# Performance work log

Hardware: AMD Instinct MI355X
Metric: run time of the kernel (lower is better)

Reference implementation:

```python
import jax, jax.numpy as jnp
import numpy as np
from jax import lax

B, C, N, COUT, H, W = 8, 64, 16, 3, 96, 96
EPS = 1e-5  # torch GroupNorm / InstanceNorm2d default eps


def group_norm(x, gamma, beta, groups):
    n, c, h, w = x.shape
    xg = x.reshape(n, groups, c // groups, h, w)
    mu = xg.mean((2, 3, 4), keepdims=True)
    var = xg.var((2, 3, 4), keepdims=True)
    xg = (xg - mu) / jnp.sqrt(var + EPS)
    return xg.reshape(n, c, h, w) * gamma[None, :, None, None] + beta[None, :, None, None]


def instance_norm(x, gamma, beta):
    mu = x.mean((2, 3), keepdims=True)
    var = x.var((2, 3), keepdims=True)
    return (x - mu) / jnp.sqrt(var + EPS) * gamma[None, :, None, None] + beta[None, :, None, None]


def conv3x3(x, w, b):
    y = lax.conv_general_dilated(x, w, (1, 1), 'SAME',
                                 dimension_numbers=('NCHW', 'OIHW', 'NCHW'))
    return y + b[None, :, None, None]


def setup_inputs() -> dict:
    key = jax.random.key(0)
    ks = jax.random.split(key, 8)
    p = {}
    p['sr'] = jax.random.normal(ks[0], (B, C, H, W), jnp.float32)
    p['tg'] = jax.random.normal(ks[1], (B, C, H, W), jnp.float32)
    # self.w : Conv2d(c, c*n, 1) -> 1x1 conv == matmul over channels
    p['w_w'] = jax.random.normal(ks[2], (C * N, C), jnp.float32) * 0.05
    p['w_b'] = jnp.zeros((C * N,), jnp.float32)
    # mask_block: GN(c//4,c), ReLU, Conv(c,64,3), GN(16,64), ReLU, Conv(64,1,3)
    p['gn1_g'] = jnp.ones((C,), jnp.float32)
    p['gn1_b'] = jnp.zeros((C,), jnp.float32)
    p['c1_w'] = jax.random.normal(ks[3], (64, C, 3, 3), jnp.float32) * 0.05
    p['c1_b'] = jnp.zeros((64,), jnp.float32)
    p['gn2_g'] = jnp.ones((64,), jnp.float32)
    p['gn2_b'] = jnp.zeros((64,), jnp.float32)
    p['c2_w'] = jax.random.normal(ks[4], (1, 64, 3, 3), jnp.float32) * 0.05
    p['c2_b'] = jnp.zeros((1,), jnp.float32)
    # gen_block: IN(n), ReLU, Conv(n,n,1), IN(n), ReLU, Conv(n,cout,1)
    p['in1_g'] = jnp.ones((N,), jnp.float32)
    p['in1_b'] = jnp.zeros((N,), jnp.float32)
    p['c3_w'] = jax.random.normal(ks[5], (N, N), jnp.float32) * 0.1
    p['c3_b'] = jnp.zeros((N,), jnp.float32)
    p['in2_g'] = jnp.ones((N,), jnp.float32)
    p['in2_b'] = jnp.zeros((N,), jnp.float32)
    p['c4_w'] = jax.random.normal(ks[6], (COUT, N), jnp.float32) * 0.1
    p['c4_b'] = jnp.zeros((COUT,), jnp.float32)
    return p


def reference(sr, tg, w_w, w_b, gn1_g, gn1_b, c1_w, c1_b, gn2_g, gn2_b,
              c2_w, c2_b, in1_g, in1_b, c3_w, c3_b, in2_g, in2_b, c4_w, c4_b):
    b, c, h, w = sr.shape
    n = N
    # 1x1 conv then view to capsule layout [b, n, c, h*w]
    s = jnp.einsum('oc,bchw->bohw', w_w, sr) + w_b[None, :, None, None]
    s = s.reshape(b, n, c, h * w)
    op = s.sum(3, keepdims=True)  # [b,n,c,1]
    cof = None
    for _ in range(3):  # fixed 3-step dynamic routing
        opn = op / jnp.maximum(jnp.linalg.norm(op, axis=2, keepdims=True), 1e-12)
        cof = jax.nn.softmax((s * opn).sum(2, keepdims=True), axis=3)  # [b,n,1,hw]
        op = (s * cof).sum(3, keepdims=True)  # [b,n,c,1]
    # broadcast capsule vectors onto target feature map
    msk_tg = (tg[:, None, :, :, :] + op[:, :, :, :, None]).reshape(b * n, c, h, w)
    x = group_norm(msk_tg, gn1_g, gn1_b, c // 4)
    x = conv3x3(jax.nn.relu(x), c1_w, c1_b)
    x = group_norm(x, gn2_g, gn2_b, 64 // 4)
    x = conv3x3(jax.nn.relu(x), c2_w, c2_b)  # [b*n,1,h,w]
    msk = x.reshape(b, n, h, w)
    # spatial center-of-mass loss
    hw_cof = jax.nn.softmax(msk.reshape(b, n, h * w), -1).reshape(b, n, h, w)[..., None]
    hw_idx = jnp.stack(jnp.meshgrid(jnp.linspace(-1.0, 1.0, h),
                                    jnp.linspace(-1.0, 1.0, w), indexing='ij'), -1)[None, None]
    hw_centr = (hw_cof * hw_idx).sum((2, 3), keepdims=True)  # [b,n,1,1,2]
    centr_loss = (hw_cof * (hw_idx - hw_centr) ** 2).sum((2, 3, 4)).mean()
    # gen_block + sigmoid activation
    g = instance_norm(msk, in1_g, in1_b)
    g = jnp.einsum('on,bnhw->bohw', c3_w, jax.nn.relu(g)) + c3_b[None, :, None, None]
    g = instance_norm(g, in2_g, in2_b)
    rec = jax.nn.sigmoid(jnp.einsum('on,bnhw->bohw', c4_w, jax.nn.relu(g)) + c4_b[None, :, None, None])
    # outer product capsule x mask: [b,n,c,1] x [b,n,h,w] -> [b,n,c,h,w]
    op_out = jnp.einsum('bnc,bnhw->bnchw', op[..., 0], msk)
    return (op_out, msk, rec, centr_loss, cof.reshape(b, n, h, w))
```

## Files before the change

kernel.cpp:

```cpp
#include <hip/hip_runtime.h>
#include <math.h>

#define BB 8
#define CC 64
#define NCAP 16
#define HH 96
#define WW 96
#define PP (HH*WW)
#define BNN (BB*NCAP)
#define EPSN 1e-5f

typedef short short8 __attribute__((ext_vector_type(8)));
typedef unsigned short u16x8 __attribute__((ext_vector_type(8)));
typedef unsigned short u16x4 __attribute__((ext_vector_type(4)));
typedef float float4v __attribute__((ext_vector_type(4)));

__device__ __forceinline__ float bf2f(unsigned short u){
  union{unsigned int i; float f;} x; x.i = ((unsigned int)u)<<16; return x.f;
}
__device__ __forceinline__ unsigned short f2bf(float f){
  union{float f; unsigned int i;} x; x.f=f;
  unsigned int r = x.i + 0x7fffu + ((x.i>>16)&1u);
  return (unsigned short)(r>>16);
}
__device__ __forceinline__ float4v mfma16(short8 a, short8 b, float4v c){
  return __builtin_amdgcn_mfma_f32_16x16x32_bf16(a, b, c, 0, 0, 0);
}

__device__ __forceinline__ float blkred_sum(float v, float* red4){
  int tid = threadIdx.x; int lane = tid & 63, wv = tid >> 6;
  #pragma unroll
  for (int off=32; off>0; off>>=1) v += __shfl_down(v, off, 64);
  __syncthreads();
  if (lane == 0) red4[wv] = v;
  __syncthreads();
  return red4[0] + red4[1] + red4[2] + red4[3];
}
__device__ __forceinline__ float blkred_max(float v, float* red4){
  int tid = threadIdx.x; int lane = tid & 63, wv = tid >> 6;
  #pragma unroll
  for (int off=32; off>0; off>>=1) v = fmaxf(v, __shfl_down(v, off, 64));
  __syncthreads();
  if (lane == 0) red4[wv] = v;
  __syncthreads();
  return fmaxf(fmaxf(red4[0], red4[1]), fmaxf(red4[2], red4[3]));
}

__global__ void kpre_tgt(const float* __restrict__ tg, unsigned short* __restrict__ tgt){
  int b = blockIdx.x/36, pc = blockIdx.x - (blockIdx.x/36)*36;
  int p = pc*256 + threadIdx.x;
  unsigned short vals[CC];
  #pragma unroll 8
  for (int c=0;c<CC;c++) vals[c] = f2bf(tg[((size_t)b*CC + c)*PP + p]);
  u16x8* dst = (u16x8*)&tgt[((size_t)b*PP + p)*CC];
  #pragma unroll
  for (int j=0;j<8;j++){
    u16x8 v;
    #pragma unroll
    for (int e=0;e<8;e++) v[e] = vals[j*8+e];
    dst[j] = v;
  }
}

__global__ void kw_bf16(const float* __restrict__ w1, unsigned short* __restrict__ Wt){
  int i = blockIdx.x*256 + threadIdx.x;
  int o = i/576; int rem = i - o*576; int c = rem/9; int tap = rem - c*9;
  Wt[(tap*CC + o)*CC + c] = f2bf(w1[i]);
}

__global__ void k0_colstats(const float* __restrict__ sr, const float* __restrict__ tg,
                            float* __restrict__ t, float* __restrict__ S1, float* __restrict__ S2){
  int row = blockIdx.x;
  const float* srp = sr + (size_t)row * PP;
  const float* tgp = tg + (size_t)row * PP;
  float s0=0.f, a1=0.f, a2=0.f;
  for (int p = threadIdx.x; p < PP; p += 256){
    s0 += srp[p];
    float v = tgp[p];
    a1 += v; a2 += v*v;
  }
  __shared__ float red4[4];
  s0 = blkred_sum(s0, red4);
  a1 = blkred_sum(a1, red4);
  a2 = blkred_sum(a2, red4);
  if (threadIdx.x == 0){ t[row]=s0; S1[row]=a1; S2[row]=a2; }
}

__global__ void k_update(const float* __restrict__ Wm, const float* __restrict__ wb,
                         const float* __restrict__ vec, float biasmul, int perB,
                         float* __restrict__ opv, float* __restrict__ uv, float* __restrict__ bu){
  int bn = blockIdx.x; int n = bn & (NCAP-1); int b = bn >> 4;
  int c = threadIdx.x;
  __shared__ float Wsh[CC*65];
  __shared__ float vsh[CC];
  __shared__ float opsh[CC];
  vsh[c] = perB ? vec[b*CC + c] : vec[bn*CC + c];
  const float* Wn = Wm + (size_t)n*CC*CC;
  for (int i=c;i<CC*CC;i+=64){ int r=i>>6, k=i&63; Wsh[r*65+k]=Wn[i]; }
  __syncthreads();
  float acc = biasmul * wb[n*CC + c];
  #pragma unroll 8
  for (int k=0;k<CC;k++) acc += Wsh[c*65+k]*vsh[k];
  opv[bn*CC+c] = acc;
  float ss = acc*acc;
  #pragma unroll
  for (int off=32;off>0;off>>=1) ss += __shfl_down(ss, off, 64);
  ss = __shfl(ss, 0, 64);
  float inv = 1.0f / fmaxf(sqrtf(ss), 1e-12f);
  opsh[c] = acc * inv;
  __syncthreads();
  float uacc = 0.f;
  #pragma unroll 8
  for (int k=0;k<CC;k++) uacc += opsh[k] * Wsh[k*65+c];
  uv[bn*CC+c] = uacc;
  float bb = opsh[c]*wb[n*CC+c];
  #pragma unroll
  for (int off=32;off>0;off>>=1) bb += __shfl_down(bb, off, 64);
  if (c==0) bu[bn] = bb;
}

__global__ __launch_bounds__(128) void k2f_dpass(
    const float* __restrict__ sr, const float* __restrict__ uv,
    const float* __restrict__ bu, float* __restrict__ dbuf,
    float* __restrict__ partm, float* __restrict__ partz,
    float* __restrict__ prt, int writed){
  int b = blockIdx.x / 72; int pc = blockIdx.x - b*72;
  int tid = threadIdx.x;
  int p = pc*128 + tid;
  __shared__ float ush[NCAP][CC];
  __shared__ float bush[NCAP];
  __shared__ float msh[NCAP];
  __shared__ float wsh[NCAP*132];
  __shared__ float srsh[CC*132];
  for (int i=tid;i<NCAP*CC;i+=128) ush[i>>6][i&63] = uv[b*NCAP*CC + i];
  if (tid < NCAP) bush[tid] = bu[b*NCAP+tid];
  __syncthreads();
  float acc[NCAP];
  #pragma unroll
  for (int n=0;n<NCAP;n++) acc[n]=bush[n];
  #pragma unroll 4
  for (int c=0;c<CC;c++){
    float v = sr[((size_t)b*CC + c)*PP + p];
    srsh[c*132+tid] = v;
    #pragma unroll
    for (int n=0;n<NCAP;n++) acc[n] += ush[n][c]*v;
  }
  #pragma unroll
  for (int n=0;n<NCAP;n++){
    wsh[n*132+tid] = acc[n];
    if (writed) dbuf[((size_t)(b*NCAP+n))*PP + p] = acc[n];
  }
  __syncthreads();
  {
    int n = tid >> 3, seg = tid & 7;
    float m = -1e30f;
    #pragma unroll
    for (int i=0;i<16;i++) m = fmaxf(m, wsh[n*132+seg*16+i]);
    #pragma unroll
    for (int off=1; off<8; off<<=1) m = fmaxf(m, __shfl_xor(m, off, 64));
    float z = 0.f;
    #pragma unroll
    for (int i=0;i<16;i++) z += __expf(wsh[n*132+seg*16+i] - m);
    #pragma unroll
    for (int off=1; off<8; off<<=1) z += __shfl_xor(z, off, 64);
    if (seg == 0){
      partm[(b*NCAP + n)*72 + pc] = m;
      partz[(b*NCAP + n)*72 + pc] = z;
      msh[n] = m;
    }
  }
  __syncthreads();
  #pragma unroll
  for (int n=0;n<NCAP;n++) wsh[n*132+tid] = __expf(wsh[n*132+tid]-msh[n]);
  __syncthreads();
  {
    int c = tid & 63, half = tid >> 6;
    float acc8[8];
    #pragma unroll
    for (int i=0;i<8;i++) acc8[i]=0.f;
    const float4* sp = (const float4*)&srsh[c*132];
    #pragma unroll 4
    for (int k=0;k<32;k++){
      float4 sv = sp[k];
      #pragma unroll
      for (int i=0;i<8;i++){
        float4 wv = *(const float4*)&wsh[(half*8+i)*132+4*k];
        acc8[i] += wv.x*sv.x + wv.y*sv.y + wv.z*sv.z + wv.w*sv.w;
      }
    }
    float* pb = prt + (((size_t)b*72+pc)*NCAP + half*8)*CC + c;
    #pragma unroll
    for (int i=0;i<8;i++) pb[(size_t)i*CC] = acc8[i];
  }
}

__global__ void k_iter(const float* __restrict__ prt, const float* __restrict__ partm,
                       const float* __restrict__ partz, const float* __restrict__ Wm,
                       const float* __restrict__ wb, float* __restrict__ mrow,
                       float* __restrict__ zrow, float* __restrict__ opv,
                       float* __restrict__ uv, float* __restrict__ bu){
  int bn = blockIdx.x; int n = bn & (NCAP-1); int b = bn >> 4;
  int c = threadIdx.x;
  float m1 = partm[bn*72 + c];
  float m2 = (c < 8) ? partm[bn*72 + 64 + c] : -1e30f;
  float mm = fmaxf(m1, m2);
  #pragma unroll
  for (int off=32;off>0;off>>=1) mm = fmaxf(mm, __shfl_xor(mm, off, 64));
  float z = partz[bn*72 + c]*__expf(m1 - mm);
  if (c < 8) z += partz[bn*72 + 64 + c]*__expf(m2 - mm);
  #pragma unroll
  for (int off=32;off>0;off>>=1) z += __shfl_xor(z, off, 64);
  if (c==0){ mrow[bn]=mm; zrow[bn]=z; }
  float invZ = 1.0f/z;
  float s = 0.f;
  #pragma unroll 8
  for (int pc=0;pc<72;pc++){
    float w = __expf(partm[bn*72+pc] - mm);
    s += prt[(((size_t)b*72+pc)*NCAP + n)*CC + c] * w;
  }
  float rvc = s*invZ;
  __shared__ float Wsh[CC*65];
  __shared__ float vsh[CC];
  __shared__ float opsh[CC];
  vsh[c] = rvc;
  const float* Wn = Wm + (size_t)n*CC*CC;
  for (int i=c;i<CC*CC;i+=64){ int r=i>>6, k=i&63; Wsh[r*65+k]=Wn[i]; }
  __syncthreads();
  float acc = wb[n*CC + c];
  #pragma unroll 8
  for (int k=0;k<CC;k++) acc += Wsh[c*65+k]*vsh[k];
  opv[bn*CC+c] = acc;
  float ss = acc*acc;
  #pragma unroll
  for (int off=32;off>0;off>>=1) ss += __shfl_down(ss, off, 64);
  ss = __shfl(ss, 0, 64);
  float inv = 1.0f / fmaxf(sqrtf(ss), 1e-12f);
  opsh[c] = acc * inv;
  __syncthreads();
  float uacc = 0.f;
  #pragma unroll 8
  for (int k=0;k<CC;k++) uacc += opsh[k] * Wsh[k*65+c];
  uv[bn*CC+c] = uacc;
  float bb = opsh[c]*wb[n*CC+c];
  #pragma unroll
  for (int off=32;off>0;off>>=1) bb += __shfl_down(bb, off, 64);
  if (c==0) bu[bn] = bb;
}

__global__ void k6_cofout(const float* __restrict__ dbuf, const float* __restrict__ mrow,
                          const float* __restrict__ zrow, float* __restrict__ cof){
  int bn = blockIdx.y;
  int p = blockIdx.x*256 + threadIdx.x;
  float m=mrow[bn], invz=1.0f/zrow[bn];
  cof[(size_t)bn*PP+p] = __expf(dbuf[(size_t)bn*PP+p]-m)*invz;
}

__global__ void k7_gn1(const float* __restrict__ S1, const float* __restrict__ S2,
                       const float* __restrict__ opv, const float* __restrict__ g1,
                       const float* __restrict__ b1, float* __restrict__ Aaff,
                       float* __restrict__ Daff, float* __restrict__ gn2s,
                       float* __restrict__ gn2q, float* __restrict__ in2s,
                       float* __restrict__ in2q, float* __restrict__ lossout){
  int bn = blockIdx.x; int b = bn >> 4;
  int c = threadIdx.x;
  __shared__ float e1[CC], e2[CC], mu[16], ri[16];
  float op = opv[bn*CC+c];
  float s1 = S1[b*CC+c], s2 = S2[b*CC+c];
  e1[c] = s1 + (float)PP*op;
  e2[c] = s2 + 2.0f*op*s1 + (float)PP*op*op;
  __syncthreads();
  if (c < 16){
    float m  = (e1[4*c]+e1[4*c+1]+e1[4*c+2]+e1[4*c+3])*(1.0f/(4.0f*PP));
    float qq = (e2[4*c]+e2[4*c+1]+e2[4*c+2]+e2[4*c+3])*(1.0f/(4.0f*PP));
    mu[c]=m; ri[c]=rsqrtf(qq-m*m+EPSN);
    gn2s[bn*16+c]=0.f; gn2q[bn*16+c]=0.f;
  }
  if (bn==0){
    in2s[c]=0.f; in2s[CC+c]=0.f; in2q[c]=0.f; in2q[CC+c]=0.f;
    if (c==0) lossout[0]=0.f;
  }
  __syncthreads();
  int g = c>>2;
  float A = ri[g]*g1[c];
  Aaff[bn*CC+c]=A;
  Daff[bn*CC+c]=(op-mu[g])*A + b1[c];
}

__global__ __launch_bounds__(256, 6) void k8_conv1_mfma(
    const unsigned short* __restrict__ tgt, const unsigned short* __restrict__ Wt,
    const float* __restrict__ c1b, const float* __restrict__ Aaff,
    const float* __restrict__ Daff, unsigned short* __restrict__ y1b,
    float* __restrict__ gn2s, float* __restrict__ gn2q){
  int blk = blockIdx.x;
  int bn = blk/72, tt = blk - bn*72;
  int ty = tt/6, tx = tt - ty*6;
  int y0 = ty*8, x0 = tx*16;
  int b = bn >> 4;
  int tid = threadIdx.x, w = tid>>6, lane = tid&63, quad = lane>>4, col16 = lane&15;

  __shared__ unsigned short xh[10*18*72];
  __shared__ float Ash[CC], Dsh[CC];
  if (tid < CC){ Ash[tid]=Aaff[bn*CC+tid]; Dsh[tid]=Daff[bn*CC+tid]; }
  __syncthreads();

  const unsigned short* tgb = tgt + (size_t)b*PP*CC;
  for (int task = tid; task < 1440; task += 256){
    int j = task & 7, pi = task >> 3;
    int row = pi/18, col = pi - row*18;
    int gy = y0 + row - 1, gx = x0 + col - 1;
    u16x8 ov;
    if ((unsigned)gy < (unsigned)HH && (unsigned)gx < (unsigned)WW){
      u16x8 iv = *(const u16x8*)(tgb + ((size_t)(gy*WW+gx))*CC + j*8);
      #pragma unroll
      for (int e=0;e<8;e++){
        float f = bf2f(iv[e]);
        f = fmaxf(Ash[j*8+e]*f + Dsh[j*8+e], 0.f);
        ov[e] = f2bf(f);
      }
    } else {
      #pragma unroll
      for (int e=0;e<8;e++) ov[e]=0;
    }
    *(u16x8*)&xh[(row*18+col)*72 + j*8] = ov;
  }
  __syncthreads();

  float4v acc[4][2];
  #pragma unroll
  for (int mt=0;mt<4;mt++)
    #pragma unroll
    for (int ri=0;ri<2;ri++)
      #pragma unroll
      for (int e=0;e<4;e++) acc[mt][ri][e]=0.f;

  const unsigned short* xb0 = &xh[((2*w)*18 + col16)*72 + quad*8];
  const unsigned short* wbase = Wt + (size_t)(col16*CC + quad*8);
  #pragma unroll
  for (int tap=0; tap<9; ++tap){
    const int dy = tap/3, dx = tap - (tap/3)*3;
    const int toff = (dy*18 + dx)*72;
    #pragma unroll
    for (int chunk=0; chunk<2; ++chunk){
      short8 a[4];
      #pragma unroll
      for (int mt=0;mt<4;mt++)
        a[mt] = *(const short8*)(wbase + tap*4096 + mt*1024 + chunk*32);
      short8 bf[2];
      #pragma unroll
      for (int ri=0;ri<2;ri++)
        bf[ri] = *(const short8*)(xb0 + toff + ri*(18*72) + chunk*32);
      #pragma unroll
      for (int mt=0;mt<4;mt++)
        #pragma unroll
        for (int ri=0;ri<2;ri++)
          acc[mt][ri] = mfma16(a[mt], bf[ri], acc[mt][ri]);
    }
  }

  __syncthreads();
  unsigned short* ybuf = xh;
  #pragma unroll
  for (int mt=0;mt<4;mt++){
    float gs=0.f, gq=0.f;
    #pragma unroll
    for (int ri=0;ri<2;ri++){
      u16x4 pv;
      #pragma unroll
      for (int e=0;e<4;e++){
        int o = mt*16 + quad*4 + e;
        float v = acc[mt][ri][e] + c1b[o];
        pv[e] = f2bf(v);
        gs += v; gq += v*v;
      }
      *(u16x4*)&ybuf[((2*w+ri)*16 + col16)*72 + mt*16 + quad*4] = pv;
    }
    #pragma unroll
    for (int off=1; off<16; off<<=1){
      gs += __shfl_xor(gs, off, 64);
      gq += __shfl_xor(gq, off, 64);
    }
    if (col16==0){
      atomicAdd(&gn2s[bn*16 + mt*4 + quad], gs);
      atomicAdd(&gn2q[bn*16 + mt*4 + quad], gq);
    }
  }
  __syncthreads();
  unsigned short* ybn = y1b + (size_t)bn*PP*CC;
  #pragma unroll
  for (int pass=0; pass<4; ++pass){
    int row = pass*2 + (tid>>7);
    int chunk = tid & 127;
    int pix = row*16 + (chunk>>3), c8 = chunk&7;
    u16x8 v = *(const u16x8*)&ybuf[pix*72 + c8*8];
    *(u16x8*)&ybn[(size_t)((y0+row)*WW + x0)*CC + chunk*8] = v;
  }
}

__global__ __launch_bounds__(256) void k10_conv2(
    const unsigned short* __restrict__ y1b, const float* __restrict__ w2,
    const float* __restrict__ b2, const float* __restrict__ gn2s,
    const float* __restrict__ gn2q, const float* __restrict__ g2c,
    const float* __restrict__ b2c, float* __restrict__ mskout){
  int blk=blockIdx.x; int bn=blk/36; int tt=blk-bn*36;
  int y0=(tt/3)*8, x0=(tt%3)*32;
  int tid=threadIdx.x;
  __shared__ unsigned short xh2[10*34*72];
  __shared__ float wsh2[CC*9];
  __shared__ float Ash[CC], Dsh[CC];
  __shared__ float mg[16], rg[16];
  for (int i=tid;i<CC*9;i+=256) wsh2[i]=w2[i];
  if (tid<16){
    float m = gn2s[bn*16+tid]*(1.0f/(4.0f*PP));
    float q = gn2q[bn*16+tid]*(1.0f/(4.0f*PP));
    mg[tid]=m; rg[tid]=rsqrtf(q-m*m+EPSN);
  }
  __syncthreads();
  if (tid<CC){
    float A = rg[tid>>2]*g2c[tid];
    Ash[tid]=A; Dsh[tid]=b2c[tid]-mg[tid>>2]*A;
  }

  const unsigned short* yb = y1b + (size_t)bn*PP*CC;
  for (int task=tid; task<2720; task+=256){
    int j = task & 7, pi = task >> 3;
    int row = pi/34, col = pi - row*34;
    int gy = y0 + row - 1, gx = x0 + col - 1;
    u16x8 iv;
    if ((unsigned)gy < (unsigned)HH && (unsigned)gx < (unsigned)WW){
      iv = *(const u16x8*)(yb + ((size_t)(gy*WW+gx))*CC + j*8);
    } else {
      #pragma unroll
      for (int e=0;e<8;e++) iv[e]=0;
    }
    *(u16x8*)&xh2[(row*34+col)*72 + j*8] = iv;
  }
  __syncthreads();

  int xi = tid&31, yi = tid>>5;
  float acc = 0.f;
  for (int t=0; t<9; ++t){
    int kh = t/3, kw = t - kh*3;
    int gy2 = y0 + yi + kh - 1, gx2 = x0 + xi + kw - 1;
    if ((unsigned)gy2 < (unsigned)HH && (unsigned)gx2 < (unsigned)WW){
      const unsigned short* px = &xh2[((yi+kh)*34 + xi+kw)*72];
      #pragma unroll
      for (int oct=0; oct<8; ++oct){
        u16x8 v = *(const u16x8*)(px + oct*8);
        #pragma unroll
        for (int e=0;e<8;e++){
          int c = oct*8 + e;
          float xv = fmaxf(Ash[c]*bf2f(v[e]) + Dsh[c], 0.f);
          acc += wsh2[c*9 + t] * xv;
        }
      }
    }
  }
  acc += b2[0];
  mskout[(size_t)bn*PP + (size_t)(y0+yi)*WW + (x0+xi)] = acc;
}

__global__ void k11_mskstats(const float* __restrict__ msk, const float* __restrict__ in1g,
                             const float* __restrict__ in1b, float* __restrict__ in1A,
                             float* __restrict__ in1D, float* __restrict__ lossout){
  int bn = blockIdx.x; int n = bn & (NCAP-1);
  const float* mp = msk + (size_t)bn*PP;
  __shared__ float red4[4];
  float mx=-1e30f, s=0.f, q=0.f;
  for (int p=threadIdx.x;p<PP;p+=256){ float v=mp[p]; mx=fmaxf(mx,v); s+=v; q+=v*v; }
  mx = blkred_max(mx, red4);
  s  = blkred_sum(s, red4);
  q  = blkred_sum(q, red4);
  float z=0.f, sy=0.f, sx=0.f, syy=0.f, sxx=0.f;
  for (int p=threadIdx.x;p<PP;p+=256){
    float e = __expf(mp[p]-mx);
    int py = p/WW, px = p - py*WW;
    float iy = -1.0f + py*(2.0f/95.0f);
    float ix = -1.0f + px*(2.0f/95.0f);
    z+=e; sy+=e*iy; sx+=e*ix; syy+=e*iy*iy; sxx+=e*ix*ix;
  }
  z=blkred_sum(z,red4); sy=blkred_sum(sy,red4); sx=blkred_sum(sx,red4);
  syy=blkred_sum(syy,red4); sxx=blkred_sum(sxx,red4);
  if (threadIdx.x==0){
    float invz=1.0f/z;
    float ey=sy*invz, ex=sx*invz;
    float lv=(syy*invz-ey*ey)+(sxx*invz-ex*ex);
    atomicAdd(lossout, lv*(1.0f/128.0f));
    float mu=s*(1.0f/PP), var=q*(1.0f/PP)-mu*mu;
    float A=rsqrtf(var+EPSN)*in1g[n];
    in1A[bn]=A; in1D[bn]=in1b[n]-mu*A;
  }
}

__global__ void k13_gen1(const float* __restrict__ msk, const float* __restrict__ in1A,
                         const float* __restrict__ in1D, const float* __restrict__ c3w,
                         const float* __restrict__ c3b, float* __restrict__ g2,
                         float* __restrict__ in2s, float* __restrict__ in2q){
  int b = blockIdx.x/36; int pc = blockIdx.x - b*36;
  int p = pc*256+threadIdx.x;
  __shared__ float wsh[NCAP*NCAP];
  __shared__ float Ash[NCAP], Dsh[NCAP], bsh[NCAP];
  if (threadIdx.x < NCAP*NCAP) wsh[threadIdx.x] = c3w[threadIdx.x];
  if (threadIdx.x < NCAP){
    Ash[threadIdx.x]=in1A[b*NCAP+threadIdx.x];
    Dsh[threadIdx.x]=in1D[b*NCAP+threadIdx.x];
    bsh[threadIdx.x]=c3b[threadIdx.x];
  }
  __syncthreads();
  float h[NCAP];
  #pragma unroll
  for (int n=0;n<NCAP;n++)
    h[n] = fmaxf(0.f, Ash[n]*msk[(size_t)(b*NCAP+n)*PP+p] + Dsh[n]);
  float g[NCAP];
  #pragma unroll
  for (int o=0;o<NCAP;o++){
    float a = bsh[o];
    #pragma unroll
    for (int n=0;n<NCAP;n++) a += wsh[o*NCAP+n]*h[n];
    g[o]=a;
    g2[(size_t)(b*NCAP+o)*PP+p]=a;
  }
  int lane = threadIdx.x & 63;
  #pragma unroll
  for (int o=0;o<NCAP;o++){
    float a=g[o], q=g[o]*g[o];
    #pragma unroll
    for (int off=32;off>0;off>>=1){ a+=__shfl_down(a,off,64); q+=__shfl_down(q,off,64); }
    if (lane==0){ atomicAdd(&in2s[b*NCAP+o],a); atomicAdd(&in2q[b*NCAP+o],q); }
  }
}

__global__ void k15_rec(const float* __restrict__ g2, const float* __restrict__ in2s,
                        const float* __restrict__ in2q, const float* __restrict__ in2g,
                        const float* __restrict__ in2b, const float* __restrict__ c4w,
                        const float* __restrict__ c4b, float* __restrict__ rec){
  int b = blockIdx.x/36; int pc = blockIdx.x - b*36;
  int p = pc*256+threadIdx.x;
  __shared__ float wsh[3*NCAP], Ash[NCAP], Dsh[NCAP], bsh[3];
  if (threadIdx.x<3*NCAP) wsh[threadIdx.x]=c4w[threadIdx.x];
  if (threadIdx.x<NCAP){
    float m=in2s[b*NCAP+threadIdx.x]*(1.0f/PP);
    float q=in2q[b*NCAP+threadIdx.x]*(1.0f/PP);
    float A=rsqrtf(q-m*m+EPSN)*in2g[threadIdx.x];
    Ash[threadIdx.x]=A; Dsh[threadIdx.x]=in2b[threadIdx.x]-m*A;
  }
  if (threadIdx.x<3) bsh[threadIdx.x]=c4b[threadIdx.x];
  __syncthreads();
  float h[NCAP];
  #pragma unroll
  for (int o=0;o<NCAP;o++)
    h[o]=fmaxf(0.f, Ash[o]*g2[(size_t)(b*NCAP+o)*PP+p]+Dsh[o]);
  #pragma unroll
  for (int j=0;j<3;j++){
    float z=bsh[j];
    #pragma unroll
    for (int o=0;o<NCAP;o++) z += wsh[j*NCAP+o]*h[o];
    rec[(size_t)(b*3+j)*PP+p] = 1.0f/(1.0f+__expf(-z));
  }
}

__global__ void k16_opout(const float* __restrict__ opv, const float* __restrict__ msk,
                          float* __restrict__ out){
  int bn = blockIdx.x / 9; int pt = blockIdx.x - bn*9;
  int base = pt*1024;
  __shared__ float ms[1024];
  __shared__ float opl[CC];
  for (int i=threadIdx.x;i<1024;i+=256) ms[i]=msk[(size_t)bn*PP+base+i];
  if (threadIdx.x<CC) opl[threadIdx.x]=opv[bn*CC+threadIdx.x];
  __syncthreads();
  float4 mv = ((const float4*)ms)[threadIdx.x];
  float* obase = out + (size_t)bn*CC*PP + base;
  #pragma unroll 4
  for (int c=0;c<CC;c++){
    float ov = opl[c];
    ((float4*)(obase + (size_t)c*PP))[threadIdx.x] = make_float4(ov*mv.x,ov*mv.y,ov*mv.z,ov*mv.w);
  }
}

extern "C" void kernel_launch(void* const* d_in, const int* in_sizes, int n_in,
                              void* d_out, int out_size, void* d_ws, size_t ws_size,
                              hipStream_t stream){
  const float* sr   = (const float*)d_in[0];
  const float* tg   = (const float*)d_in[1];
  const float* w_w  = (const float*)d_in[2];
  const float* w_b  = (const float*)d_in[3];
  const float* gn1g = (const float*)d_in[4];
  const float* gn1b = (const float*)d_in[5];
  const float* c1w  = (const float*)d_in[6];
  const float* c1b  = (const float*)d_in[7];
  const float* gn2g = (const float*)d_in[8];
  const float* gn2b = (const float*)d_in[9];
  const float* c2w  = (const float*)d_in[10];
  const float* c2b  = (const float*)d_in[11];
  const float* in1g = (const float*)d_in[12];
  const float* in1b = (const float*)d_in[13];
  const float* c3w  = (const float*)d_in[14];
  const float* c3b  = (const float*)d_in[15];
  const float* in2g = (const float*)d_in[16];
  const float* in2b = (const float*)d_in[17];
  const float* c4w  = (const float*)d_in[18];
  const float* c4b  = (const float*)d_in[19];
  float* out = (float*)d_out;
  float* ws  = (float*)d_ws;

  float* t_   = ws + 0;
  float* S1   = ws + 512;
  float* S2   = ws + 1024;
  float* opv  = ws + 1536;
  float* uv   = ws + 9728;
  float* bu   = ws + 17920;
  float* mrow = ws + 18048;
  float* zrow = ws + 18176;
  float* Aaff = ws + 26496;
  float* Daff = ws + 34688;
  float* gn2s = ws + 42880;
  float* gn2q = ws + 44928;
  float* in1A = ws + 63360;
  float* in1D = ws + 63488;
  float* in2s = ws + 63744;
  float* in2q = ws + 63872;
  float* dbuf = ws + 65536;
  float* g2   = ws + 65536 + 1179648;

  unsigned short* y1b = (unsigned short*)d_out;
  unsigned short* tgt = (unsigned short*)((char*)d_out + 150994944);
  unsigned short* Wt  = (unsigned short*)((char*)d_out + 160432128);
  float* prt   = (float*)((char*)d_out + 160505856);
  float* partm = (float*)((char*)d_out + 162865152);
  float* partz = (float*)((char*)d_out + 162902016);
  float* mskout  = out + 75497472;
  float* recout  = out + 76677120;
  float* lossout = out + 76898304;
  float* cofout  = out + 76898305;

  kpre_tgt<<<BB*36, 256, 0, stream>>>(tg, tgt);
  kw_bf16<<<144, 256, 0, stream>>>(c1w, Wt);
  k0_colstats<<<BB*CC, 256, 0, stream>>>(sr, tg, t_, S1, S2);
  k_update<<<BNN, 64, 0, stream>>>(w_w, w_b, t_, (float)PP, 1, opv, uv, bu);
  for (int it=0; it<3; ++it){
    k2f_dpass<<<BB*72, 128, 0, stream>>>(sr, uv, bu, dbuf, partm, partz, prt, it==2 ? 1 : 0);
    k_iter<<<BNN, 64, 0, stream>>>(prt, partm, partz, w_w, w_b, mrow, zrow, opv, uv, bu);
  }
  k6_cofout<<<dim3(36, BNN), 256, 0, stream>>>(dbuf, mrow, zrow, cofout);
  k7_gn1<<<BNN, 64, 0, stream>>>(S1, S2, opv, gn1g, gn1b, Aaff, Daff, gn2s, gn2q, in2s, in2q, lossout);
  k8_conv1_mfma<<<BNN*72, 256, 0, stream>>>(tgt, Wt, c1b, Aaff, Daff, y1b, gn2s, gn2q);
  k10_conv2<<<BNN*36, 256, 0, stream>>>(y1b, c2w, c2b, gn2s, gn2q, gn2g, gn2b, mskout);
  k11_mskstats<<<BNN, 256, 0, stream>>>(mskout, in1g, in1b, in1A, in1D, lossout);
  k13_gen1<<<BB*36, 256, 0, stream>>>(mskout, in1A, in1D, c3w, c3b, g2, in2s, in2q);
  k15_rec<<<BB*36, 256, 0, stream>>>(g2, in2s, in2q, in2g, in2b, c4w, c4b, recout);
  k16_opout<<<BNN*9, 256, 0, stream>>>(opv, mskout, out);
}
```

Baseline: 1.203 ms.

## Enlarge conv1 tile to 8x32 with channel-split halo staging and direct stores

The 3x3 conv1 MFMA kernel now covers an 8x32 pixel tile per block instead of 8x16, doubling accumulators per wave to improve weight-fragment reuse and halve the block count. The input halo is staged in two 32-channel halves to keep the shared-memory footprint small, and the block index is remapped so consecutive blocks share the same batch image. Outputs are written straight from registers to global memory instead of going through a shared-memory transpose. In exchange, register pressure rises (occupancy hint lowered to 5), there are extra barriers, and the direct stores are 8-byte scattered writes rather than coalesced 16-byte ones.

Result: slower. 1.310 ms (+8.8%).

```diff
diff --git a/kernel.cpp b/kernel.cpp
--- a/kernel.cpp
+++ b/kernel.cpp
@@ -286,93 +286,102 @@
   Daff[bn*CC+c]=(op-mu[g])*A + b1[c];
 }
 
-__global__ __launch_bounds__(256, 6) void k8_conv1_mfma(
+__global__ __launch_bounds__(256, 5) void k8_conv1_mfma(
     const unsigned short* __restrict__ tgt, const unsigned short* __restrict__ Wt,
     const float* __restrict__ c1b, const float* __restrict__ Aaff,
     const float* __restrict__ Daff, unsigned short* __restrict__ y1b,
     float* __restrict__ gn2s, float* __restrict__ gn2q){
-  int blk = blockIdx.x;
-  int bn = blk/72, tt = blk - bn*72;
-  int ty = tt/6, tx = tt - ty*6;
-  int y0 = ty*8, x0 = tx*16;
-  int b = bn >> 4;
+  int bid = blockIdx.x;
+  int b   = bid & 7;
+  int rem = bid >> 3;
+  int n   = rem / 36;
+  int tt  = rem - n*36;
+  int bn  = (b<<4) | n;
+  int ty = tt/3, tx = tt - ty*3;
+  int y0 = ty*8, x0 = tx*32;
   int tid = threadIdx.x, w = tid>>6, lane = tid&63, quad = lane>>4, col16 = lane&15;
 
-  __shared__ unsigned short xh[10*18*72];
+  __shared__ unsigned short xh[10*34*32];
   __shared__ float Ash[CC], Dsh[CC];
   if (tid < CC){ Ash[tid]=Aaff[bn*CC+tid]; Dsh[tid]=Daff[bn*CC+tid]; }
-  __syncthreads();
+
+  float4v acc[4][4];
+  #pragma unroll
+  for (int mt=0;mt<4;mt++)
+    #pragma unroll
+    for (int nt=0;nt<4;nt++)
+      #pragma unroll
+      for (int e=0;e<4;e++) acc[mt][nt][e]=0.f;
 
   const unsigned short* tgb = tgt + (size_t)b*PP*CC;
-  for (int task = tid; task < 1440; task += 256){
-    int j = task & 7, pi = task >> 3;
-    int row = pi/18, col = pi - row*18;
-    int gy = y0 + row - 1, gx = x0 + col - 1;
-    u16x8 ov;
-    if ((unsigned)gy < (unsigned)HH && (unsigned)gx < (unsigned)WW){
-      u16x8 iv = *(const u16x8*)(tgb + ((size_t)(gy*WW+gx))*CC + j*8);
-      #pragma unroll
-      for (int e=0;e<8;e++){
-        float f = bf2f(iv[e]);
-        f = fmaxf(Ash[j*8+e]*f + Dsh[j*8+e], 0.f);
-        ov[e] = f2bf(f);
+  const unsigned short* wb0 = Wt + (size_t)(col16*CC + quad*8);
+
+  #pragma unroll 1
+  for (int half=0; half<2; ++half){
+    __syncthreads();
+    for (int task = tid; task < 1360; task += 256){
+      int j = task & 3, pi = task >> 2;
+      int row = pi/34, col = pi - row*34;
+      int gy = y0 + row - 1, gx = x0 + col - 1;
+      u16x8 ov;
+      if ((unsigned)gy < (unsigned)HH && (unsigned)gx < (unsigned)WW){
+        u16x8 iv = *(const u16x8*)(tgb + ((size_t)(gy*WW+gx))*CC + half*32 + j*8);
+        #pragma unroll
+        for (int e=0;e<8;e++){
+          int cch = half*32 + j*8 + e;
+          float f = bf2f(iv[e]);
+          f = fmaxf(Ash[cch]*f + Dsh[cch], 0.f);
+          ov[e] = f2bf(f);
+        }
+      } else {
+        #pragma unroll
+        for (int e=0;e<8;e++) ov[e]=0;
       }
-    } else {
-      #pragma unroll
-      for (int e=0;e<8;e++) ov[e]=0;
-    }
-    *(u16x8*)&xh[(row*18+col)*72 + j*8] = ov;
-  }
-  __syncthreads();
-
-  float4v acc[4][2];
-  #pragma unroll
-  for (int mt=0;mt<4;mt++)
-    #pragma unroll
-    for (int ri=0;ri<2;ri++)
-      #pragma unroll
-      for (int e=0;e<4;e++) acc[mt][ri][e]=0.f;
-
-  const unsigned short* xb0 = &xh[((2*w)*18 + col16)*72 + quad*8];
-  const unsigned short* wbase = Wt + (size_t)(col16*CC + quad*8);
-  #pragma unroll
-  for (int tap=0; tap<9; ++tap){
-    const int dy = tap/3, dx = tap - (tap/3)*3;
-    const int toff = (dy*18 + dx)*72;
-    #pragma unroll
-    for (int chunk=0; chunk<2; ++chunk){
+      *(u16x8*)&xh[pi*32 + j*8] = ov;
+    }
+    __syncthreads();
+
+    const unsigned short* xb0 = &xh[((2*w + 1)*34 + 1 + col16)*32 + quad*8];
+    const unsigned short* wbase = wb0 + half*32;
+    #pragma unroll
+    for (int tap=0; tap<9; ++tap){
+      const int dy = tap/3 - 1, dx = tap - (tap/3)*3 - 1;
+      const int toff = (dy*34 + dx)*32;
       short8 a[4];
       #pragma unroll
       for (int mt=0;mt<4;mt++)
-        a[mt] = *(const short8*)(wbase + tap*4096 + mt*1024 + chunk*32);
-      short8 bf[2];
-      #pragma unroll
-      for (int ri=0;ri<2;ri++)
-        bf[ri] = *(const short8*)(xb0 + toff + ri*(18*72) + chunk*32);
+        a[mt] = *(const short8*)(wbase + tap*4096 + mt*1024);
+      short8 bf[4];
+      #pragma unroll
+      for (int nt=0;nt<4;nt++){
+        int ri = nt>>1, h = nt&1;
+        bf[nt] = *(const short8*)(xb0 + toff + ri*(34*32) + h*(16*32));
+      }
       #pragma unroll
       for (int mt=0;mt<4;mt++)
         #pragma unroll
-        for (int ri=0;ri<2;ri++)
-          acc[mt][ri] = mfma16(a[mt], bf[ri], acc[mt][ri]);
-    }
-  }
-
-  __syncthreads();
-  unsigned short* ybuf = xh;
+        for (int nt=0;nt<4;nt++)
+          acc[mt][nt] = mfma16(a[mt], bf[nt], acc[mt][nt]);
+    }
+  }
+
+  unsigned short* ybn = y1b + (size_t)bn*PP*CC;
   #pragma unroll
   for (int mt=0;mt<4;mt++){
     float gs=0.f, gq=0.f;
     #pragma unroll
-    for (int ri=0;ri<2;ri++){
+    for (int nt=0;nt<4;nt++){
+      int ri = nt>>1, h = nt&1;
+      int y = y0 + 2*w + ri, x = x0 + h*16 + col16;
       u16x4 pv;
       #pragma unroll
       for (int e=0;e<4;e++){
         int o = mt*16 + quad*4 + e;
-        float v = acc[mt][ri][e] + c1b[o];
+        float v = acc[mt][nt][e] + c1b[o];
         pv[e] = f2bf(v);
         gs += v; gq += v*v;
       }
-      *(u16x4*)&ybuf[((2*w+ri)*16 + col16)*72 + mt*16 + quad*4] = pv;
+      *(u16x4*)&ybn[(size_t)(y*WW + x)*CC + mt*16 + quad*4] = pv;
     }
     #pragma unroll
     for (int off=1; off<16; off<<=1){
@@ -383,16 +392,6 @@
       atomicAdd(&gn2s[bn*16 + mt*4 + quad], gs);
       atomicAdd(&gn2q[bn*16 + mt*4 + quad], gq);
     }
-  }
-  __syncthreads();
-  unsigned short* ybn = y1b + (size_t)bn*PP*CC;
-  #pragma unroll
-  for (int pass=0; pass<4; ++pass){
-    int row = pass*2 + (tid>>7);
-    int chunk = tid & 127;
-    int pix = row*16 + (chunk>>3), c8 = chunk&7;
-    u16x8 v = *(const u16x8*)&ybuf[pix*72 + c8*8];
-    *(u16x8*)&ybn[(size_t)((y0+row)*WW + x0)*CC + chunk*8] = v;
   }
 }
 
@@ -642,7 +641,7 @@
   }
   k6_cofout<<<dim3(36, BNN), 256, 0, stream>>>(dbuf, mrow, zrow, cofout);
   k7_gn1<<<BNN, 64, 0, stream>>>(S1, S2, opv, gn1g, gn1b, Aaff, Daff, gn2s, gn2q, in2s, in2q, lossout);
-  k8_conv1_mfma<<<BNN*72, 256, 0, stream>>>(tgt, Wt, c1b, Aaff, Daff, y1b, gn2s, gn2q);
+  k8_conv1_mfma<<<BNN*36, 256, 0, stream>>>(tgt, Wt, c1b, Aaff, Daff, y1b, gn2s, gn2q);
   k10_conv2<<<BNN*36, 256, 0, stream>>>(y1b, c2w, c2b, gn2s, gn2q, gn2g, gn2b, mskout);
   k11_mskstats<<<BNN, 256, 0, stream>>>(mskout, in1g, in1b, in1A, in1D, lossout);
   k13_gen1<<<BB*36, 256, 0, stream>>>(mskout, in1A, in1D, c3w, c3b, g2, in2s, in2q);
```
